# Kernel optimization log

Hardware: AMD Instinct MI355X
Metric: run time of the kernel (lower is better)

The kernel has to match this reference:

```python
import math
import jax, jax.numpy as jnp
from jax import lax
import numpy as np

B_, H_, W_, C_ = 4, 64, 64, 96
DSTATE, DCONV, EXPAND = 16, 3, 2.0
DI = int(EXPAND * C_)            # d_inner = 192
RANK = math.ceil(C_ / 16)        # dt_rank = 6
K = 4                            # 4 scan directions


def setup_inputs() -> dict:
    key = jax.random.key(0)
    ks = jax.random.split(key, 8)
    x = jax.random.normal(ks[0], (B_, H_, W_, C_), jnp.float32)
    in_proj_w = jax.random.normal(ks[1], (2 * DI, C_), jnp.float32) * 0.02
    conv_w = jax.random.normal(ks[2], (DI, 1, DCONV, DCONV), jnp.float32) * 0.1
    conv_b = jnp.zeros((DI,), jnp.float32)
    x_proj_w = jax.random.normal(ks[3], (K, RANK + 2 * DSTATE, DI), jnp.float32) * 0.02
    dt_std = RANK ** -0.5
    dt_projs_w = jax.random.uniform(ks[4], (K, DI, RANK), jnp.float32, -dt_std, dt_std)
    # inverse-softplus init of dt bias, as in dt_init
    dt = jnp.exp(jax.random.uniform(ks[5], (K, DI), jnp.float32)
                 * (math.log(0.1) - math.log(1e-3)) + math.log(1e-3))
    dt = jnp.clip(dt, 1e-4, None)
    dt_projs_b = dt + jnp.log(-jnp.expm1(-dt))
    A_logs = jnp.log(jnp.tile(jnp.arange(1, DSTATE + 1, dtype=jnp.float32)[None, :], (K * DI, 1)))
    Ds = jnp.ones((K * DI,), jnp.float32)
    ln_g = jnp.ones((DI,), jnp.float32)
    ln_b = jnp.zeros((DI,), jnp.float32)
    out_proj_w = jax.random.normal(ks[6], (C_, DI), jnp.float32) * 0.02
    return dict(x=x, in_proj_w=in_proj_w, conv_w=conv_w, conv_b=conv_b,
                x_proj_w=x_proj_w, dt_projs_w=dt_projs_w, dt_projs_b=dt_projs_b,
                A_logs=A_logs, Ds=Ds, ln_g=ln_g, ln_b=ln_b, out_proj_w=out_proj_w)


def reference(x, in_proj_w, conv_w, conv_b, x_proj_w, dt_projs_w, dt_projs_b,
              A_logs, Ds, ln_g, ln_b, out_proj_w):
    B, H, W, C = x.shape
    Di, N, L = DI, DSTATE, H * W
    # in_proj -> x, z gate
    xz = jnp.einsum('bhwc,ec->bhwe', x, in_proj_w)
    xh, z = jnp.split(xz, 2, axis=-1)
    # depthwise 3x3 conv + SiLU (NCHW)
    xc = jnp.transpose(xh, (0, 3, 1, 2))
    xc = lax.conv_general_dilated(xc, conv_w, (1, 1), 'SAME', feature_group_count=Di)
    xc = jax.nn.silu(xc + conv_b[None, :, None, None])
    # 4 directional sequences: hw, wh(transposed), and their reverses
    x_flat = xc.reshape(B, Di, L)
    x_tr = jnp.transpose(xc, (0, 1, 3, 2)).reshape(B, Di, L)
    x_hwwh = jnp.stack([x_flat, x_tr], axis=1)                 # B,2,Di,L
    xs = jnp.concatenate([x_hwwh, jnp.flip(x_hwwh, axis=-1)], axis=1)  # B,K,Di,L
    # projections for dt, B, C
    x_dbl = jnp.einsum('bkdl,kcd->bkcl', xs, x_proj_w)
    dts = x_dbl[:, :, :RANK]
    Bs = x_dbl[:, :, RANK:RANK + N]            # B,K,N,L
    Cs = x_dbl[:, :, RANK + N:]                # B,K,N,L
    dts = jnp.einsum('bkrl,kdr->bkdl', dts, dt_projs_w)
    delta = jax.nn.softplus(dts + dt_projs_b[None, :, :, None])  # B,K,Di,L
    A = -jnp.exp(A_logs).reshape(K, Di, N)
    # selective scan over L (sequential recurrence, vectorized over B,K,Di,N)
    u_l = jnp.transpose(xs, (3, 0, 1, 2))      # L,B,K,Di
    d_l = jnp.transpose(delta, (3, 0, 1, 2))   # L,B,K,Di
    B_l = jnp.transpose(Bs, (3, 0, 1, 2))      # L,B,K,N
    C_l = jnp.transpose(Cs, (3, 0, 1, 2))      # L,B,K,N

    def step(h, inp):
        u_t, d_t, b_t, c_t = inp
        dA = jnp.exp(d_t[..., None] * A[None])                  # B,K,Di,N
        h = h * dA + (d_t * u_t)[..., None] * b_t[:, :, None, :]
        y = jnp.einsum('bkdn,bkn->bkd', h, c_t)
        return h, y

    h0 = jnp.zeros((B, K, Di, N), xs.dtype)
    _, ys = lax.scan(step, h0, (u_l, d_l, B_l, C_l))            # L,B,K,Di
    out_y = jnp.transpose(ys, (1, 2, 3, 0)) + xs * Ds.reshape(K, Di)[None, :, :, None]
    # undo direction permutations and sum the 4 streams
    inv_y = jnp.flip(out_y[:, 2:4], axis=-1)
    wh_y = jnp.transpose(out_y[:, 1].reshape(B, Di, W, H), (0, 1, 3, 2)).reshape(B, Di, L)
    invwh_y = jnp.transpose(inv_y[:, 1].reshape(B, Di, W, H), (0, 1, 3, 2)).reshape(B, Di, L)
    y = out_y[:, 0] + inv_y[:, 0] + wh_y + invwh_y              # B,Di,L
    y = jnp.transpose(y, (0, 2, 1)).reshape(B, H, W, Di)
    # out_norm (LayerNorm), gate with SiLU(z), out_proj
    mu = jnp.mean(y, axis=-1, keepdims=True)
    var = jnp.mean(jnp.square(y - mu), axis=-1, keepdims=True)
    y = (y - mu) * lax.rsqrt(var + 1e-5) * ln_g + ln_b
    y = y * jax.nn.silu(z)
    return jnp.einsum('bhwd,cd->bhwc', y, out_proj_w)
```

## Files before the change

### kernel.cpp

```cpp
#include <hip/hip_runtime.h>
#include <math.h>

#define DI 192
#define NS 16
#define LL 4096
#define NC 128
#define CH 32

__device__ __forceinline__ float siluf(float x) {
  return x / (1.f + __expf(-x));
}

__device__ __forceinline__ int row_l(int k, int p) {
  const int q = (k >= 2) ? (4095 - p) : p;
  return (k & 1) ? (((q & 63) << 6) | (q >> 6)) : q;
}

__device__ __forceinline__ int row_stride(int k) {
  return (k == 0) ? 1 : (k == 1) ? 64 : (k == 2) ? -1 : -64;
}

__device__ __forceinline__ void decays16(float w, float* dec) {
  const float w2 = w * w, w4 = w2 * w2, w8 = w4 * w4;
  const float w3 = w2 * w, w5 = w4 * w, w6 = w4 * w2, w7 = w4 * w3;
  dec[0] = w;  dec[1] = w2; dec[2] = w3; dec[3] = w4;
  dec[4] = w5; dec[5] = w6; dec[6] = w7; dec[7] = w8;
  dec[8] = w8 * w;  dec[9] = w8 * w2; dec[10] = w8 * w3; dec[11] = w8 * w4;
  dec[12] = w8 * w5; dec[13] = w8 * w6; dec[14] = w8 * w7; dec[15] = w8 * w8;
}

__device__ __forceinline__ void softplus_w(float x, float& dl, float& w) {
  const float e = __expf(x);
  dl = __logf(1.f + e);
  w = __builtin_amdgcn_rcpf(1.f + e);
}

__global__ __launch_bounds__(256) void k_inproj(
    const float* __restrict__ x, const float* __restrict__ w,
    float* __restrict__ xh, float* __restrict__ z) {
  __shared__ float As[64 * 97];
  __shared__ float Bs[64 * 97];
  const int t = threadIdx.x;
  const int bm = blockIdx.x, bn = blockIdx.y;
  const float* xrow = x + (size_t)bm * 64 * 96;
  const float* wrow = w + (size_t)bn * 64 * 96;
#pragma unroll
  for (int rep = 0; rep < 6; ++rep) {
    int fi = rep * 256 + t;
    int r = fi / 24, kq = (fi - r * 24) * 4;
    float4 av = *reinterpret_cast<const float4*>(xrow + r * 96 + kq);
    As[r * 97 + kq + 0] = av.x; As[r * 97 + kq + 1] = av.y;
    As[r * 97 + kq + 2] = av.z; As[r * 97 + kq + 3] = av.w;
    float4 bv = *reinterpret_cast<const float4*>(wrow + r * 96 + kq);
    Bs[r * 97 + kq + 0] = bv.x; Bs[r * 97 + kq + 1] = bv.y;
    Bs[r * 97 + kq + 2] = bv.z; Bs[r * 97 + kq + 3] = bv.w;
  }
  __syncthreads();
  const int tm = (t >> 4) * 4, tn = (t & 15) * 4;
  float acc[4][4] = {};
  for (int kk = 0; kk < 96; ++kk) {
    float av[4], bv[4];
#pragma unroll
    for (int i = 0; i < 4; ++i) av[i] = As[(tm + i) * 97 + kk];
#pragma unroll
    for (int j = 0; j < 4; ++j) bv[j] = Bs[(tn + j) * 97 + kk];
#pragma unroll
    for (int i = 0; i < 4; ++i)
#pragma unroll
      for (int j = 0; j < 4; ++j) acc[i][j] += av[i] * bv[j];
  }
  const int e0 = bn * 64 + tn;
#pragma unroll
  for (int i = 0; i < 4; ++i) {
    size_t m = (size_t)bm * 64 + tm + i;
    float4 v = make_float4(acc[i][0], acc[i][1], acc[i][2], acc[i][3]);
    if (e0 < DI) *reinterpret_cast<float4*>(xh + m * DI + e0) = v;
    else         *reinterpret_cast<float4*>(z + m * DI + (e0 - DI)) = v;
  }
}

__global__ __launch_bounds__(192) void k_conv(
    const float* __restrict__ xh, const float* __restrict__ cw,
    const float* __restrict__ cb, float* __restrict__ uT0) {
  __shared__ float tile[DI * 65];
  const int h = blockIdx.x, b = blockIdx.y;
  const int d = threadIdx.x;
  float wgt[9];
#pragma unroll
  for (int i = 0; i < 9; ++i) wgt[i] = cw[d * 9 + i];
  const float bias = cb[d];
  const bool hm = (h > 0), hp = (h < 63);
  const float* rowm = xh + ((size_t)(b * 64 + (h - 1)) * 64) * DI + d;
  const float* row0 = xh + ((size_t)(b * 64 + h) * 64) * DI + d;
  const float* rowp = xh + ((size_t)(b * 64 + (h + 1)) * 64) * DI + d;
  float cp0 = 0.f, cp1 = 0.f, cp2 = 0.f;
  float cc0 = hm ? rowm[0] : 0.f;
  float cc1 = row0[0];
  float cc2 = hp ? rowp[0] : 0.f;
  for (int w = 0; w < 64; ++w) {
    float cn0 = 0.f, cn1 = 0.f, cn2 = 0.f;
    if (w < 63) {
      cn0 = hm ? rowm[(w + 1) * DI] : 0.f;
      cn1 = row0[(w + 1) * DI];
      cn2 = hp ? rowp[(w + 1) * DI] : 0.f;
    }
    float acc = bias
      + cp0 * wgt[0] + cc0 * wgt[1] + cn0 * wgt[2]
      + cp1 * wgt[3] + cc1 * wgt[4] + cn1 * wgt[5]
      + cp2 * wgt[6] + cc2 * wgt[7] + cn2 * wgt[8];
    tile[d * 65 + w] = siluf(acc);
    cp0 = cc0; cp1 = cc1; cp2 = cc2;
    cc0 = cn0; cc1 = cn1; cc2 = cn2;
  }
  __syncthreads();
  for (int w = 0; w < 64; ++w) {
    uT0[((size_t)((b * 64 + h) * 64 + w)) * DI + d] = tile[d * 65 + w];
  }
}

__global__ __launch_bounds__(256, 2) void k_xdbl(
    const float* __restrict__ uT0, const float* __restrict__ xpw,
    float* __restrict__ xdbl) {
  __shared__ float X[DI * 64];
  __shared__ float Wl[40 * DI];
  const int cblk = blockIdx.x, k = blockIdx.y, b = blockIdx.z;
  const int t = threadIdx.x;
  {
    const float4* wsrc = reinterpret_cast<const float4*>(xpw + (size_t)k * 38 * DI);
    float4* wdst = reinterpret_cast<float4*>(Wl);
#pragma unroll
    for (int r = 0; r < 8; ++r) {
      int q = r * 256 + t;
      if (q < 1920) wdst[q] = (q < 1824) ? wsrc[q] : make_float4(0.f, 0.f, 0.f, 0.f);
    }
  }
  {
    const int i = t >> 2, q = t & 3;
    const float* urow = uT0 + ((size_t)b * LL + row_l(k, cblk * 64 + i)) * DI;
    const float4* urow4 = reinterpret_cast<const float4*>(urow);
#pragma unroll
    for (int dd = 0; dd < 12; ++dd) {
      float4 v = urow4[dd * 4 + q];
      const int d0 = (dd * 4 + q) * 4;
      X[(d0 + 0) * 64 + i] = v.x;
      X[(d0 + 1) * 64 + i] = v.y;
      X[(d0 + 2) * 64 + i] = v.z;
      X[(d0 + 3) * 64 + i] = v.w;
    }
  }
  __syncthreads();
  const int c2 = t & 31, g = t >> 5;
  float acc[5][2];
#pragma unroll
  for (int j = 0; j < 5; ++j) { acc[j][0] = 0.f; acc[j][1] = 0.f; }
  for (int dq = 0; dq < 48; ++dq) {
    float4 w[5];
#pragma unroll
    for (int j = 0; j < 5; ++j)
      w[j] = *reinterpret_cast<const float4*>(&Wl[(g * 5 + j) * DI + dq * 4]);
    float x0[4], x1[4];
#pragma unroll
    for (int e = 0; e < 4; ++e) {
      x0[e] = X[(dq * 4 + e) * 64 + c2];
      x1[e] = X[(dq * 4 + e) * 64 + c2 + 32];
    }
#pragma unroll
    for (int j = 0; j < 5; ++j) {
      acc[j][0] += w[j].x * x0[0] + w[j].y * x0[1] + w[j].z * x0[2] + w[j].w * x0[3];
      acc[j][1] += w[j].x * x1[0] + w[j].y * x1[1] + w[j].z * x1[2] + w[j].w * x1[3];
    }
  }
  __syncthreads();
  float* O = X;
#pragma unroll
  for (int j = 0; j < 5; ++j) {
    const int co = g * 5 + j;
    O[(c2 +  0) * 40 + co] = acc[j][0];
    O[(c2 + 32) * 40 + co] = acc[j][1];
  }
  __syncthreads();
  {
    const int bk = b * 4 + k;
    const float4* O4 = reinterpret_cast<const float4*>(O);
    float4* dst4 = reinterpret_cast<float4*>(xdbl + ((size_t)(bk * 64 + cblk) * 64) * 40);
#pragma unroll
    for (int r = 0; r < 3; ++r) {
      int idx = r * 256 + t;
      if (idx < 640) dst4[idx] = O4[idx];
    }
  }
}

__global__ __launch_bounds__(192, 6) void k_scan1(
    const float* __restrict__ uT0, const float* __restrict__ xdbl,
    const float* __restrict__ dtw, const float* __restrict__ dtb,
    float* __restrict__ hbuf, float* __restrict__ sumd) {
  __shared__ float Sl[CH * 40];
  const int c = blockIdx.x, k = blockIdx.y, b = blockIdx.z;
  const int d = threadIdx.x;
  const int kd = k * DI + d;
  const int bk = b * 4 + k;
  {
    const float4* src4 = reinterpret_cast<const float4*>(
        xdbl + ((size_t)bk * LL + c * CH) * 40);
    float4* dst4 = reinterpret_cast<float4*>(Sl);
#pragma unroll
    for (int r = 0; r < 2; ++r) {
      int idx = r * 192 + d;
      if (idx < 320) dst4[idx] = src4[idx];
    }
  }
  float wdt[6];
#pragma unroll
  for (int r = 0; r < 6; ++r) wdt[r] = dtw[kd * 6 + r];
  const float bdt = dtb[kd];
  float h[NS];
#pragma unroll
  for (int n = 0; n < NS; ++n) h[n] = 0.f;
  float sd = 0.f;
  __syncthreads();
  const ptrdiff_t dr = (ptrdiff_t)row_stride(k) * DI;
  const float* up = uT0 + ((size_t)b * LL + row_l(k, c * CH)) * DI + d;
  float uA = *up;
  for (int i = 0; i < CH; ++i) {
    const float uB = (i + 1 < CH) ? up[dr] : 0.f;
    const float* Sr = &Sl[i * 40];
    const float4 q0 = *reinterpret_cast<const float4*>(Sr + 0);
    const float4 q1 = *reinterpret_cast<const float4*>(Sr + 4);
    const float4 q2 = *reinterpret_cast<const float4*>(Sr + 8);
    const float4 q3 = *reinterpret_cast<const float4*>(Sr + 12);
    const float4 q4 = *reinterpret_cast<const float4*>(Sr + 16);
    const float4 q5 = *reinterpret_cast<const float4*>(Sr + 20);
    const float dl0 = bdt + q0.x * wdt[0] + q0.y * wdt[1] + q0.z * wdt[2]
                          + q0.w * wdt[3] + q1.x * wdt[4] + q1.y * wdt[5];
    float dl, w;
    softplus_w(dl0, dl, w);
    sd += dl;
    const float du = dl * uA;
    float dec[NS];
    decays16(w, dec);
    const float fB[16] = {q1.z, q1.w, q2.x, q2.y, q2.z, q2.w, q3.x, q3.y,
                          q3.z, q3.w, q4.x, q4.y, q4.z, q4.w, q5.x, q5.y};
#pragma unroll
    for (int n = 0; n < NS; ++n)
      h[n] = h[n] * dec[n] + du * fB[n];
    up += dr;
    uA = uB;
  }
  const size_t hb = (size_t)(bk * NC + c) * NS;
#pragma unroll
  for (int n = 0; n < NS; ++n) hbuf[(hb + n) * DI + d] = h[n];
  sumd[(size_t)(bk * NC + c) * DI + d] = sd;
}

__global__ __launch_bounds__(256, 2) void k_scan2(
    const float* __restrict__ sumd, float* __restrict__ hbuf) {
  const int bid = blockIdx.x;
  const int bk = bid / 12, r = bid % 12;
  const int n = (r / 3) * 4 + (threadIdx.x >> 6);
  const int d = (r % 3) * 64 + (threadIdx.x & 63);
  const float An = -(float)(n + 1);
  float h = 0.f;
#define HIDX(cc) (((size_t)(bk * NC + (cc)) * NS + n) * DI + d)
#define SIDX(cc) ((size_t)(bk * NC + (cc)) * DI + d)
  float hA = hbuf[HIDX(0)], sA = sumd[SIDX(0)];
  float hB, sB;
  for (int cc = 0; cc < NC; cc += 2) {
    hB = hbuf[HIDX(cc + 1)]; sB = sumd[SIDX(cc + 1)];
    {
      const float wdec = __expf(An * sA);
      hbuf[HIDX(cc)] = h;
      h = h * wdec + hA;
    }
    if (cc + 2 < NC) { hA = hbuf[HIDX(cc + 2)]; sA = sumd[SIDX(cc + 2)]; }
    {
      const float wdec = __expf(An * sB);
      hbuf[HIDX(cc + 1)] = h;
      h = h * wdec + hB;
    }
  }
#undef HIDX
#undef SIDX
}

template <bool ACCUM>
__global__ __launch_bounds__(192, 4) void k_scan3(
    const float* __restrict__ uT0, const float* __restrict__ xdbl,
    const float* __restrict__ dtw, const float* __restrict__ dtb,
    const float* __restrict__ hbuf,
    const float* __restrict__ Dsv, int kbase,
    float* __restrict__ yb0, float* __restrict__ yb1,
    float* __restrict__ yb2, float* __restrict__ yb3) {
  __shared__ float Sl[CH * 40];
  const int c = blockIdx.x, b = blockIdx.z;
  const int k = kbase + (int)blockIdx.y;
  const int d = threadIdx.x;
  const int kd = k * DI + d;
  const int bk = b * 4 + k;
  float* ybuf = (k == 0) ? yb0 : (k == 1) ? yb1 : (k == 2) ? yb2 : yb3;
  {
    const float4* src4 = reinterpret_cast<const float4*>(
        xdbl + ((size_t)bk * LL + c * CH) * 40);
    float4* dst4 = reinterpret_cast<float4*>(Sl);
#pragma unroll
    for (int r = 0; r < 2; ++r) {
      int idx = r * 192 + d;
      if (idx < 320) dst4[idx] = src4[idx];
    }
  }
  float wdt[6];
#pragma unroll
  for (int r = 0; r < 6; ++r) wdt[r] = dtw[kd * 6 + r];
  const float bdt = dtb[kd];
  const float Dv = Dsv[kd];
  float h[NS];
  {
    const size_t hb = (size_t)(bk * NC + c) * NS;
#pragma unroll
    for (int n = 0; n < NS; ++n) h[n] = hbuf[(hb + n) * DI + d];
  }
  __syncthreads();
  const ptrdiff_t dr = (ptrdiff_t)row_stride(k) * DI;
  const size_t base = ((size_t)b * LL + row_l(k, c * CH)) * DI + d;
  const float* up = uT0 + base;
  float* yp = ybuf + base;
  float uA = *up;
  float yoA = ACCUM ? *yp : 0.f;
  for (int i = 0; i < CH; ++i) {
    float uB = 0.f, yoB = 0.f;
    if (i + 1 < CH) {
      uB = up[dr];
      if (ACCUM) yoB = yp[dr];
    }
    const float* Sr = &Sl[i * 40];
    const float4 q0 = *reinterpret_cast<const float4*>(Sr + 0);
    const float4 q1 = *reinterpret_cast<const float4*>(Sr + 4);
    const float4 q2 = *reinterpret_cast<const float4*>(Sr + 8);
    const float4 q3 = *reinterpret_cast<const float4*>(Sr + 12);
    const float4 q4 = *reinterpret_cast<const float4*>(Sr + 16);
    const float4 q5 = *reinterpret_cast<const float4*>(Sr + 20);
    const float4 q6 = *reinterpret_cast<const float4*>(Sr + 24);
    const float4 q7 = *reinterpret_cast<const float4*>(Sr + 28);
    const float4 q8 = *reinterpret_cast<const float4*>(Sr + 32);
    const float4 q9 = *reinterpret_cast<const float4*>(Sr + 36);
    const float dl0 = bdt + q0.x * wdt[0] + q0.y * wdt[1] + q0.z * wdt[2]
                          + q0.w * wdt[3] + q1.x * wdt[4] + q1.y * wdt[5];
    float dl, w;
    softplus_w(dl0, dl, w);
    const float du = dl * uA;
    float yv = Dv * uA;
    float dec[NS];
    decays16(w, dec);
    const float fB[16] = {q1.z, q1.w, q2.x, q2.y, q2.z, q2.w, q3.x, q3.y,
                          q3.z, q3.w, q4.x, q4.y, q4.z, q4.w, q5.x, q5.y};
    const float fC[16] = {q5.z, q5.w, q6.x, q6.y, q6.z, q6.w, q7.x, q7.y,
                          q7.z, q7.w, q8.x, q8.y, q8.z, q8.w, q9.x, q9.y};
#pragma unroll
    for (int n = 0; n < NS; ++n) {
      h[n] = h[n] * dec[n] + du * fB[n];
      yv += h[n] * fC[n];
    }
    if (ACCUM) *yp = yoA + yv;
    else       *yp = yv;
    up += dr; yp += dr;
    uA = uB; yoA = yoB;
  }
}

__global__ __launch_bounds__(256) void k_lnout(
    const float* __restrict__ y0, const float* __restrict__ y1,
    const float* __restrict__ y2, const float* __restrict__ y3,
    int ny,
    const float* __restrict__ z,
    const float* __restrict__ lng, const float* __restrict__ lnb,
    const float* __restrict__ opw, float* __restrict__ out) {
  __shared__ float ytile[64 * 193];
  __shared__ float Wl[96 * DI];
  const int pt = blockIdx.x, b = blockIdx.y;
  const int t = threadIdx.x;
  {
    const float4* wsrc = reinterpret_cast<const float4*>(opw);
    float4* wdst = reinterpret_cast<float4*>(Wl);
#pragma unroll
    for (int r = 0; r < 18; ++r) wdst[r * 256 + t] = wsrc[r * 256 + t];
  }
  {
    const int c = t >> 2, q = t & 3;
    const size_t row = ((size_t)b * LL + pt * 64 + c) * DI;
    const float4* r0 = reinterpret_cast<const float4*>(y0 + row);
    const float4* r1 = reinterpret_cast<const float4*>(y1 + row);
    const float4* r2 = reinterpret_cast<const float4*>(y2 + row);
    const float4* r3 = reinterpret_cast<const float4*>(y3 + row);
#pragma unroll
    for (int dd = 0; dd < 12; ++dd) {
      float4 a = r0[dd * 4 + q];
      float4 bb = r1[dd * 4 + q];
      float vx = a.x + bb.x, vy = a.y + bb.y, vz = a.z + bb.z, vw = a.w + bb.w;
      if (ny == 4) {
        float4 cvv = r2[dd * 4 + q];
        float4 dv = r3[dd * 4 + q];
        vx += cvv.x + dv.x; vy += cvv.y + dv.y;
        vz += cvv.z + dv.z; vw += cvv.w + dv.w;
      }
      const int d0 = (dd * 4 + q) * 4;
      ytile[c * 193 + d0 + 0] = vx;
      ytile[c * 193 + d0 + 1] = vy;
      ytile[c * 193 + d0 + 2] = vz;
      ytile[c * 193 + d0 + 3] = vw;
    }
  }
  __syncthreads();
  {
    const int p = t >> 2, qq = t & 3;
    float s = 0.f, s2 = 0.f;
    for (int j = 0; j < 48; ++j) {
      float v = ytile[p * 193 + qq * 48 + j];
      s += v; s2 += v * v;
    }
    s += __shfl_xor(s, 1, 64);  s += __shfl_xor(s, 2, 64);
    s2 += __shfl_xor(s2, 1, 64); s2 += __shfl_xor(s2, 2, 64);
    const float mu = s * (1.f / 192.f);
    const float var = s2 * (1.f / 192.f) - mu * mu;
    const float rstd = rsqrtf(var + 1e-5f);
    const size_t prow = ((size_t)b * LL + pt * 64 + p) * DI;
    for (int j = 0; j < 48; ++j) {
      int d = qq * 48 + j;
      float v = (ytile[p * 193 + d] - mu) * rstd * lng[d] + lnb[d];
      float zv = z[prow + d];
      v *= siluf(zv);
      ytile[p * 193 + d] = v;
    }
  }
  __syncthreads();
  float acc[24];
#pragma unroll
  for (int j = 0; j < 24; ++j) acc[j] = 0.f;
  const int p2 = t & 63, gq = t >> 6;
  for (int dq = 0; dq < 48; ++dq) {
    float xv[4];
#pragma unroll
    for (int e = 0; e < 4; ++e) xv[e] = ytile[p2 * 193 + dq * 4 + e];
#pragma unroll
    for (int j = 0; j < 24; ++j) {
      const float4 wv = *reinterpret_cast<const float4*>(&Wl[(gq * 24 + j) * DI + dq * 4]);
      acc[j] += wv.x * xv[0] + wv.y * xv[1] + wv.z * xv[2] + wv.w * xv[3];
    }
  }
  __syncthreads();
  float* l2 = ytile;
#pragma unroll
  for (int j = 0; j < 24; ++j) l2[p2 * 97 + gq * 24 + j] = acc[j];
  __syncthreads();
  for (int rr = 0; rr < 24; ++rr) {
    int idx = rr * 256 + t;
    int pp = idx / 96, cc = idx - pp * 96;
    out[((size_t)b * LL + pt * 64 + pp) * 96 + cc] = l2[pp * 97 + cc];
  }
}

extern "C" void kernel_launch(void* const* d_in, const int* in_sizes, int n_in,
                              void* d_out, int out_size, void* d_ws, size_t ws_size,
                              hipStream_t stream) {
  const float* x          = (const float*)d_in[0];
  const float* in_proj_w  = (const float*)d_in[1];
  const float* conv_w     = (const float*)d_in[2];
  const float* conv_b     = (const float*)d_in[3];
  const float* x_proj_w   = (const float*)d_in[4];
  const float* dt_projs_w = (const float*)d_in[5];
  const float* dt_projs_b = (const float*)d_in[6];
  const float* Ds         = (const float*)d_in[8];
  const float* ln_g       = (const float*)d_in[9];
  const float* ln_b       = (const float*)d_in[10];
  const float* out_proj_w = (const float*)d_in[11];
  float* out = (float*)d_out;
  float* ws = (float*)d_ws;
  float* xh   = ws;
  float* z    = ws +  3145728;
  float* uT0  = ws +  6291456;
  float* xdbl = ws +  9437184;
  float* hbuf = ws + 12058624;
  float* y1   = ws + 18350080;
  float* y2   = ws + 21495808;
  float* y3   = ws + 24641536;
  float* sumd = xh;
  float* y0   = xh;
  const bool planA = ws_size >= (size_t)27787264 * 4;

  k_inproj<<<dim3(256, 6), dim3(256), 0, stream>>>(x, in_proj_w, xh, z);
  k_conv<<<dim3(64, 4), dim3(192), 0, stream>>>(xh, conv_w, conv_b, uT0);
  k_xdbl<<<dim3(64, 4, 4), dim3(256), 0, stream>>>(uT0, x_proj_w, xdbl);
  k_scan1<<<dim3(NC, 4, 4), dim3(192), 0, stream>>>(uT0, xdbl,
      dt_projs_w, dt_projs_b, hbuf, sumd);
  k_scan2<<<dim3(192), dim3(256), 0, stream>>>(sumd, hbuf);
  if (planA) {
    k_scan3<false><<<dim3(NC, 4, 4), dim3(192), 0, stream>>>(uT0, xdbl,
        dt_projs_w, dt_projs_b, hbuf, Ds, 0, y0, y1, y2, y3);
    k_lnout<<<dim3(64, 4), dim3(256), 0, stream>>>(y0, y1, y2, y3, 4, z,
        ln_g, ln_b, out_proj_w, out);
  } else {
    k_scan3<false><<<dim3(NC, 2, 4), dim3(192), 0, stream>>>(uT0, xdbl,
        dt_projs_w, dt_projs_b, hbuf, Ds, 0, y0, y1, y0, y1);
    k_scan3<true><<<dim3(NC, 2, 4), dim3(192), 0, stream>>>(uT0, xdbl,
        dt_projs_w, dt_projs_b, hbuf, Ds, 2, y0, y1, y0, y1);
    k_lnout<<<dim3(64, 4), dim3(256), 0, stream>>>(y0, y1, y0, y1, 2, z,
        ln_g, ln_b, out_proj_w, out);
  }
}
```

Measured before the change: 220.2 us.

## Stream scan records from global into registers with double buffering, drop LDS staging

The chunked scan kernels no longer stage the per-chunk x_dbl records into shared memory behind a barrier. Each thread now loads the records for the next step straight from global into a register double buffer while it computes the current step, and the u and y prefetch is widened to match. k_scan3 splits the C-dot into four partial sums to shorten the dependency chain, and k_scan2 prefetches four chunks at a time instead of two. The cost is higher register pressure, reflected in lower launch-bounds occupancy, and redundant per-thread global loads of the same broadcast data, which rely on caching.

```diff
diff --git a/kernel.cpp b/kernel.cpp
--- a/kernel.cpp
+++ b/kernel.cpp
@@ -191,25 +191,16 @@
   }
 }
 
-__global__ __launch_bounds__(192, 6) void k_scan1(
+__global__ __launch_bounds__(192, 5) void k_scan1(
     const float* __restrict__ uT0, const float* __restrict__ xdbl,
     const float* __restrict__ dtw, const float* __restrict__ dtb,
     float* __restrict__ hbuf, float* __restrict__ sumd) {
-  __shared__ float Sl[CH * 40];
   const int c = blockIdx.x, k = blockIdx.y, b = blockIdx.z;
   const int d = threadIdx.x;
   const int kd = k * DI + d;
   const int bk = b * 4 + k;
-  {
-    const float4* src4 = reinterpret_cast<const float4*>(
-        xdbl + ((size_t)bk * LL + c * CH) * 40);
-    float4* dst4 = reinterpret_cast<float4*>(Sl);
-#pragma unroll
-    for (int r = 0; r < 2; ++r) {
-      int idx = r * 192 + d;
-      if (idx < 320) dst4[idx] = src4[idx];
-    }
-  }
+  const float4* Rp = reinterpret_cast<const float4*>(
+      xdbl + ((size_t)bk * LL + c * CH) * 40);
   float wdt[6];
 #pragma unroll
   for (int r = 0; r < 6; ++r) wdt[r] = dtw[kd * 6 + r];
@@ -218,35 +209,47 @@
 #pragma unroll
   for (int n = 0; n < NS; ++n) h[n] = 0.f;
   float sd = 0.f;
-  __syncthreads();
   const ptrdiff_t dr = (ptrdiff_t)row_stride(k) * DI;
   const float* up = uT0 + ((size_t)b * LL + row_l(k, c * CH)) * DI + d;
-  float uA = *up;
-  for (int i = 0; i < CH; ++i) {
-    const float uB = (i + 1 < CH) ? up[dr] : 0.f;
-    const float* Sr = &Sl[i * 40];
-    const float4 q0 = *reinterpret_cast<const float4*>(Sr + 0);
-    const float4 q1 = *reinterpret_cast<const float4*>(Sr + 4);
-    const float4 q2 = *reinterpret_cast<const float4*>(Sr + 8);
-    const float4 q3 = *reinterpret_cast<const float4*>(Sr + 12);
-    const float4 q4 = *reinterpret_cast<const float4*>(Sr + 16);
-    const float4 q5 = *reinterpret_cast<const float4*>(Sr + 20);
-    const float dl0 = bdt + q0.x * wdt[0] + q0.y * wdt[1] + q0.z * wdt[2]
-                          + q0.w * wdt[3] + q1.x * wdt[4] + q1.y * wdt[5];
-    float dl, w;
-    softplus_w(dl0, dl, w);
-    sd += dl;
-    const float du = dl * uA;
-    float dec[NS];
-    decays16(w, dec);
-    const float fB[16] = {q1.z, q1.w, q2.x, q2.y, q2.z, q2.w, q3.x, q3.y,
-                          q3.z, q3.w, q4.x, q4.y, q4.z, q4.w, q5.x, q5.y};
-#pragma unroll
-    for (int n = 0; n < NS; ++n)
-      h[n] = h[n] * dec[n] + du * fB[n];
-    up += dr;
-    uA = uB;
-  }
+  float recA[24], recB[24];
+
+#define LOADR1(dst, ii) do {                                           \
+    _Pragma("unroll")                                                  \
+    for (int q = 0; q < 6; ++q)                                        \
+      *reinterpret_cast<float4*>(&dst[q * 4]) = Rp[(ii) * 10 + q];     \
+  } while (0)
+
+#define STEP1(rec, uu) do {                                            \
+    const float s0_ = bdt + rec[0] * wdt[0] + rec[1] * wdt[1]          \
+                          + rec[2] * wdt[2];                           \
+    const float s1_ = rec[3] * wdt[3] + rec[4] * wdt[4]                \
+                    + rec[5] * wdt[5];                                 \
+    float dl, w;                                                       \
+    softplus_w(s0_ + s1_, dl, w);                                      \
+    sd += dl;                                                          \
+    const float du = dl * (uu);                                        \
+    float dec[NS];                                                     \
+    decays16(w, dec);                                                  \
+    _Pragma("unroll")                                                  \
+    for (int n = 0; n < NS; ++n)                                       \
+      h[n] = h[n] * dec[n] + du * rec[6 + n];                          \
+  } while (0)
+
+  LOADR1(recA, 0);
+  float u0 = up[0];
+  float u1 = up[dr];
+  for (int i = 0; i < CH; i += 2) {
+    if (i + 1 < CH) LOADR1(recB, i + 1);
+    float un0 = (i + 2 < CH) ? up[2 * dr] : 0.f;
+    STEP1(recA, u0);
+    if (i + 2 < CH) LOADR1(recA, i + 2);
+    float un1 = (i + 3 < CH) ? up[3 * dr] : 0.f;
+    STEP1(recB, u1);
+    u0 = un0; u1 = un1; up += 2 * dr;
+  }
+#undef LOADR1
+#undef STEP1
+
   const size_t hb = (size_t)(bk * NC + c) * NS;
 #pragma unroll
   for (int n = 0; n < NS; ++n) hbuf[(hb + n) * DI + d] = h[n];
@@ -263,51 +266,49 @@
   float h = 0.f;
 #define HIDX(cc) (((size_t)(bk * NC + (cc)) * NS + n) * DI + d)
 #define SIDX(cc) ((size_t)(bk * NC + (cc)) * DI + d)
-  float hA = hbuf[HIDX(0)], sA = sumd[SIDX(0)];
-  float hB, sB;
-  for (int cc = 0; cc < NC; cc += 2) {
-    hB = hbuf[HIDX(cc + 1)]; sB = sumd[SIDX(cc + 1)];
-    {
-      const float wdec = __expf(An * sA);
-      hbuf[HIDX(cc)] = h;
-      h = h * wdec + hA;
-    }
-    if (cc + 2 < NC) { hA = hbuf[HIDX(cc + 2)]; sA = sumd[SIDX(cc + 2)]; }
-    {
-      const float wdec = __expf(An * sB);
-      hbuf[HIDX(cc + 1)] = h;
-      h = h * wdec + hB;
-    }
+  float hA[4], sA[4];
+#pragma unroll
+  for (int j = 0; j < 4; ++j) { hA[j] = hbuf[HIDX(j)]; sA[j] = sumd[SIDX(j)]; }
+  for (int cc = 0; cc < NC; cc += 4) {
+    float hB[4], sB[4];
+    if (cc + 4 < NC) {
+#pragma unroll
+      for (int j = 0; j < 4; ++j) {
+        hB[j] = hbuf[HIDX(cc + 4 + j)];
+        sB[j] = sumd[SIDX(cc + 4 + j)];
+      }
+    }
+    float wd[4];
+#pragma unroll
+    for (int j = 0; j < 4; ++j) wd[j] = __expf(An * sA[j]);
+#pragma unroll
+    for (int j = 0; j < 4; ++j) {
+      hbuf[HIDX(cc + j)] = h;
+      h = h * wd[j] + hA[j];
+    }
+#pragma unroll
+    for (int j = 0; j < 4; ++j) { hA[j] = hB[j]; sA[j] = sB[j]; }
   }
 #undef HIDX
 #undef SIDX
 }
 
 template <bool ACCUM>
-__global__ __launch_bounds__(192, 4) void k_scan3(
+__global__ __launch_bounds__(192, 3) void k_scan3(
     const float* __restrict__ uT0, const float* __restrict__ xdbl,
     const float* __restrict__ dtw, const float* __restrict__ dtb,
     const float* __restrict__ hbuf,
     const float* __restrict__ Dsv, int kbase,
     float* __restrict__ yb0, float* __restrict__ yb1,
     float* __restrict__ yb2, float* __restrict__ yb3) {
-  __shared__ float Sl[CH * 40];
   const int c = blockIdx.x, b = blockIdx.z;
   const int k = kbase + (int)blockIdx.y;
   const int d = threadIdx.x;
   const int kd = k * DI + d;
   const int bk = b * 4 + k;
   float* ybuf = (k == 0) ? yb0 : (k == 1) ? yb1 : (k == 2) ? yb2 : yb3;
-  {
-    const float4* src4 = reinterpret_cast<const float4*>(
-        xdbl + ((size_t)bk * LL + c * CH) * 40);
-    float4* dst4 = reinterpret_cast<float4*>(Sl);
-#pragma unroll
-    for (int r = 0; r < 2; ++r) {
-      int idx = r * 192 + d;
-      if (idx < 320) dst4[idx] = src4[idx];
-    }
-  }
+  const float4* Rp = reinterpret_cast<const float4*>(
+      xdbl + ((size_t)bk * LL + c * CH) * 40);
   float wdt[6];
 #pragma unroll
   for (int r = 0; r < 6; ++r) wdt[r] = dtw[kd * 6 + r];
@@ -319,52 +320,61 @@
 #pragma unroll
     for (int n = 0; n < NS; ++n) h[n] = hbuf[(hb + n) * DI + d];
   }
-  __syncthreads();
   const ptrdiff_t dr = (ptrdiff_t)row_stride(k) * DI;
   const size_t base = ((size_t)b * LL + row_l(k, c * CH)) * DI + d;
   const float* up = uT0 + base;
   float* yp = ybuf + base;
-  float uA = *up;
-  float yoA = ACCUM ? *yp : 0.f;
-  for (int i = 0; i < CH; ++i) {
-    float uB = 0.f, yoB = 0.f;
-    if (i + 1 < CH) {
-      uB = up[dr];
-      if (ACCUM) yoB = yp[dr];
-    }
-    const float* Sr = &Sl[i * 40];
-    const float4 q0 = *reinterpret_cast<const float4*>(Sr + 0);
-    const float4 q1 = *reinterpret_cast<const float4*>(Sr + 4);
-    const float4 q2 = *reinterpret_cast<const float4*>(Sr + 8);
-    const float4 q3 = *reinterpret_cast<const float4*>(Sr + 12);
-    const float4 q4 = *reinterpret_cast<const float4*>(Sr + 16);
-    const float4 q5 = *reinterpret_cast<const float4*>(Sr + 20);
-    const float4 q6 = *reinterpret_cast<const float4*>(Sr + 24);
-    const float4 q7 = *reinterpret_cast<const float4*>(Sr + 28);
-    const float4 q8 = *reinterpret_cast<const float4*>(Sr + 32);
-    const float4 q9 = *reinterpret_cast<const float4*>(Sr + 36);
-    const float dl0 = bdt + q0.x * wdt[0] + q0.y * wdt[1] + q0.z * wdt[2]
-                          + q0.w * wdt[3] + q1.x * wdt[4] + q1.y * wdt[5];
-    float dl, w;
-    softplus_w(dl0, dl, w);
-    const float du = dl * uA;
-    float yv = Dv * uA;
-    float dec[NS];
-    decays16(w, dec);
-    const float fB[16] = {q1.z, q1.w, q2.x, q2.y, q2.z, q2.w, q3.x, q3.y,
-                          q3.z, q3.w, q4.x, q4.y, q4.z, q4.w, q5.x, q5.y};
-    const float fC[16] = {q5.z, q5.w, q6.x, q6.y, q6.z, q6.w, q7.x, q7.y,
-                          q7.z, q7.w, q8.x, q8.y, q8.z, q8.w, q9.x, q9.y};
-#pragma unroll
-    for (int n = 0; n < NS; ++n) {
-      h[n] = h[n] * dec[n] + du * fB[n];
-      yv += h[n] * fC[n];
-    }
-    if (ACCUM) *yp = yoA + yv;
-    else       *yp = yv;
-    up += dr; yp += dr;
-    uA = uB; yoA = yoB;
-  }
+  float recA[40], recB[40];
+
+#define LOADR3(dst, ii) do {                                           \
+    _Pragma("unroll")                                                  \
+    for (int q = 0; q < 10; ++q)                                       \
+      *reinterpret_cast<float4*>(&dst[q * 4]) = Rp[(ii) * 10 + q];     \
+  } while (0)
+
+#define STEP3(rec, uu, yo, yoff) do {                                  \
+    const float s0_ = bdt + rec[0] * wdt[0] + rec[1] * wdt[1]          \
+                          + rec[2] * wdt[2];                           \
+    const float s1_ = rec[3] * wdt[3] + rec[4] * wdt[4]                \
+                    + rec[5] * wdt[5];                                 \
+    float dl, w;                                                       \
+    softplus_w(s0_ + s1_, dl, w);                                      \
+    const float du = dl * (uu);                                        \
+    float dec[NS];                                                     \
+    decays16(w, dec);                                                  \
+    float yv0 = Dv * (uu), yv1 = 0.f, yv2 = 0.f, yv3 = 0.f;            \
+    _Pragma("unroll")                                                  \
+    for (int n = 0; n < NS; ++n) {                                     \
+      h[n] = h[n] * dec[n] + du * rec[6 + n];                          \
+      const float t_ = h[n] * rec[22 + n];                             \
+      if ((n & 3) == 0) yv0 += t_;                                     \
+      else if ((n & 3) == 1) yv1 += t_;                                \
+      else if ((n & 3) == 2) yv2 += t_;                                \
+      else yv3 += t_;                                                  \
+    }                                                                  \
+    const float yv_ = (yv0 + yv1) + (yv2 + yv3);                       \
+    yp[yoff] = ACCUM ? ((yo) + yv_) : yv_;                             \
+  } while (0)
+
+  LOADR3(recA, 0);
+  float u0 = up[0];
+  float u1 = up[dr];
+  float yo0 = ACCUM ? yp[0] : 0.f;
+  float yo1 = ACCUM ? yp[dr] : 0.f;
+  for (int i = 0; i < CH; i += 2) {
+    if (i + 1 < CH) LOADR3(recB, i + 1);
+    float un0 = 0.f, yn0 = 0.f;
+    if (i + 2 < CH) { un0 = up[2 * dr]; if (ACCUM) yn0 = yp[2 * dr]; }
+    STEP3(recA, u0, yo0, 0);
+    if (i + 2 < CH) LOADR3(recA, i + 2);
+    float un1 = 0.f, yn1 = 0.f;
+    if (i + 3 < CH) { un1 = up[3 * dr]; if (ACCUM) yn1 = yp[3 * dr]; }
+    STEP3(recB, u1, yo1, dr);
+    u0 = un0; u1 = un1; yo0 = yn0; yo1 = yn1;
+    up += 2 * dr; yp += 2 * dr;
+  }
+#undef LOADR3
+#undef STEP3
 }
 
 __global__ __launch_bounds__(256) void k_lnout(
```

After: 243.8 us. 1.11x slower.

## Map one wave per chunk covering all channels in scan kernels

Applied to the files above, without the earlier changes.

Restructures the chunked scan kernels so that each 64-lane wavefront handles one chunk and processes three channels per lane, with four chunks per 256-thread block. Each lane reads the shared B/C/dt row once and reuses it across its three channels, which cuts LDS reads and per-block staging overhead. The output reduction is split into four partial sums to shorten the dependency chain, and the inter-chunk scan2 prefetches four chunks ahead. In exchange, register pressure rises (three 16-entry state vectors per thread), which lowers occupancy and leaves fewer blocks to spread across CUs.

```diff
diff --git a/kernel.cpp b/kernel.cpp
--- a/kernel.cpp
+++ b/kernel.cpp
@@ -191,66 +191,84 @@
   }
 }
 
-__global__ __launch_bounds__(192, 6) void k_scan1(
+#define SCAN_QLOAD6(Sr)                                                \
+    const float4 q0 = *reinterpret_cast<const float4*>((Sr) + 0);      \
+    const float4 q1 = *reinterpret_cast<const float4*>((Sr) + 4);      \
+    const float4 q2 = *reinterpret_cast<const float4*>((Sr) + 8);      \
+    const float4 q3 = *reinterpret_cast<const float4*>((Sr) + 12);     \
+    const float4 q4 = *reinterpret_cast<const float4*>((Sr) + 16);     \
+    const float4 q5 = *reinterpret_cast<const float4*>((Sr) + 20);
+
+__global__ __launch_bounds__(256, 3) void k_scan1(
     const float* __restrict__ uT0, const float* __restrict__ xdbl,
     const float* __restrict__ dtw, const float* __restrict__ dtb,
     float* __restrict__ hbuf, float* __restrict__ sumd) {
-  __shared__ float Sl[CH * 40];
-  const int c = blockIdx.x, k = blockIdx.y, b = blockIdx.z;
-  const int d = threadIdx.x;
-  const int kd = k * DI + d;
+  __shared__ float Sl[4][CH * 40];
+  const int cblk = blockIdx.x, k = blockIdx.y, b = blockIdx.z;
+  const int wv = threadIdx.x >> 6, lane = threadIdx.x & 63;
+  const int c = cblk * 4 + wv;
   const int bk = b * 4 + k;
   {
-    const float4* src4 = reinterpret_cast<const float4*>(
+    const float4* src = reinterpret_cast<const float4*>(
         xdbl + ((size_t)bk * LL + c * CH) * 40);
-    float4* dst4 = reinterpret_cast<float4*>(Sl);
-#pragma unroll
-    for (int r = 0; r < 2; ++r) {
-      int idx = r * 192 + d;
-      if (idx < 320) dst4[idx] = src4[idx];
-    }
-  }
-  float wdt[6];
-#pragma unroll
-  for (int r = 0; r < 6; ++r) wdt[r] = dtw[kd * 6 + r];
-  const float bdt = dtb[kd];
-  float h[NS];
-#pragma unroll
-  for (int n = 0; n < NS; ++n) h[n] = 0.f;
-  float sd = 0.f;
+    float4* dst = reinterpret_cast<float4*>(Sl[wv]);
+#pragma unroll
+    for (int r = 0; r < 5; ++r) dst[r * 64 + lane] = src[r * 64 + lane];
+  }
+  float wdt[3][6], bdt[3];
+#pragma unroll
+  for (int s = 0; s < 3; ++s) {
+    const int kd = k * DI + lane + 64 * s;
+#pragma unroll
+    for (int r = 0; r < 6; ++r) wdt[s][r] = dtw[kd * 6 + r];
+    bdt[s] = dtb[kd];
+  }
+  float h[3][NS];
+#pragma unroll
+  for (int s = 0; s < 3; ++s)
+#pragma unroll
+    for (int n = 0; n < NS; ++n) h[s][n] = 0.f;
+  float sd[3] = {0.f, 0.f, 0.f};
   __syncthreads();
   const ptrdiff_t dr = (ptrdiff_t)row_stride(k) * DI;
-  const float* up = uT0 + ((size_t)b * LL + row_l(k, c * CH)) * DI + d;
-  float uA = *up;
+  const float* up = uT0 + ((size_t)b * LL + row_l(k, c * CH)) * DI + lane;
+  float u0 = up[0], u1 = up[64], u2 = up[128];
   for (int i = 0; i < CH; ++i) {
-    const float uB = (i + 1 < CH) ? up[dr] : 0.f;
-    const float* Sr = &Sl[i * 40];
-    const float4 q0 = *reinterpret_cast<const float4*>(Sr + 0);
-    const float4 q1 = *reinterpret_cast<const float4*>(Sr + 4);
-    const float4 q2 = *reinterpret_cast<const float4*>(Sr + 8);
-    const float4 q3 = *reinterpret_cast<const float4*>(Sr + 12);
-    const float4 q4 = *reinterpret_cast<const float4*>(Sr + 16);
-    const float4 q5 = *reinterpret_cast<const float4*>(Sr + 20);
-    const float dl0 = bdt + q0.x * wdt[0] + q0.y * wdt[1] + q0.z * wdt[2]
-                          + q0.w * wdt[3] + q1.x * wdt[4] + q1.y * wdt[5];
-    float dl, w;
-    softplus_w(dl0, dl, w);
-    sd += dl;
-    const float du = dl * uA;
-    float dec[NS];
-    decays16(w, dec);
+    float un0 = 0.f, un1 = 0.f, un2 = 0.f;
+    if (i + 1 < CH) { un0 = up[dr]; un1 = up[dr + 64]; un2 = up[dr + 128]; }
+    const float* Sr = &Sl[wv][i * 40];
+    SCAN_QLOAD6(Sr)
     const float fB[16] = {q1.z, q1.w, q2.x, q2.y, q2.z, q2.w, q3.x, q3.y,
                           q3.z, q3.w, q4.x, q4.y, q4.z, q4.w, q5.x, q5.y};
-#pragma unroll
-    for (int n = 0; n < NS; ++n)
-      h[n] = h[n] * dec[n] + du * fB[n];
+    const float uu[3] = {u0, u1, u2};
+#pragma unroll
+    for (int s = 0; s < 3; ++s) {
+      const float dl0 = bdt[s] + q0.x * wdt[s][0] + q0.y * wdt[s][1]
+          + q0.z * wdt[s][2] + q0.w * wdt[s][3] + q1.x * wdt[s][4]
+          + q1.y * wdt[s][5];
+      float dl, w;
+      softplus_w(dl0, dl, w);
+      sd[s] += dl;
+      const float du = dl * uu[s];
+      float dec[NS];
+      decays16(w, dec);
+#pragma unroll
+      for (int n = 0; n < NS; ++n)
+        h[s][n] = h[s][n] * dec[n] + du * fB[n];
+    }
     up += dr;
-    uA = uB;
+    u0 = un0; u1 = un1; u2 = un2;
   }
   const size_t hb = (size_t)(bk * NC + c) * NS;
 #pragma unroll
-  for (int n = 0; n < NS; ++n) hbuf[(hb + n) * DI + d] = h[n];
-  sumd[(size_t)(bk * NC + c) * DI + d] = sd;
+  for (int n = 0; n < NS; ++n) {
+#pragma unroll
+    for (int s = 0; s < 3; ++s)
+      hbuf[(hb + n) * DI + lane + 64 * s] = h[s][n];
+  }
+#pragma unroll
+  for (int s = 0; s < 3; ++s)
+    sumd[(size_t)(bk * NC + c) * DI + lane + 64 * s] = sd[s];
 }
 
 __global__ __launch_bounds__(256, 2) void k_scan2(
@@ -263,107 +281,120 @@
   float h = 0.f;
 #define HIDX(cc) (((size_t)(bk * NC + (cc)) * NS + n) * DI + d)
 #define SIDX(cc) ((size_t)(bk * NC + (cc)) * DI + d)
-  float hA = hbuf[HIDX(0)], sA = sumd[SIDX(0)];
-  float hB, sB;
-  for (int cc = 0; cc < NC; cc += 2) {
-    hB = hbuf[HIDX(cc + 1)]; sB = sumd[SIDX(cc + 1)];
-    {
-      const float wdec = __expf(An * sA);
-      hbuf[HIDX(cc)] = h;
-      h = h * wdec + hA;
-    }
-    if (cc + 2 < NC) { hA = hbuf[HIDX(cc + 2)]; sA = sumd[SIDX(cc + 2)]; }
-    {
-      const float wdec = __expf(An * sB);
-      hbuf[HIDX(cc + 1)] = h;
-      h = h * wdec + hB;
-    }
+  float hA[4], sA[4];
+#pragma unroll
+  for (int j = 0; j < 4; ++j) { hA[j] = hbuf[HIDX(j)]; sA[j] = sumd[SIDX(j)]; }
+  for (int cc = 0; cc < NC; cc += 4) {
+    float hB[4], sB[4];
+    if (cc + 4 < NC) {
+#pragma unroll
+      for (int j = 0; j < 4; ++j) {
+        hB[j] = hbuf[HIDX(cc + 4 + j)];
+        sB[j] = sumd[SIDX(cc + 4 + j)];
+      }
+    }
+    float wd[4];
+#pragma unroll
+    for (int j = 0; j < 4; ++j) wd[j] = __expf(An * sA[j]);
+#pragma unroll
+    for (int j = 0; j < 4; ++j) {
+      hbuf[HIDX(cc + j)] = h;
+      h = h * wd[j] + hA[j];
+    }
+#pragma unroll
+    for (int j = 0; j < 4; ++j) { hA[j] = hB[j]; sA[j] = sB[j]; }
   }
 #undef HIDX
 #undef SIDX
 }
 
 template <bool ACCUM>
-__global__ __launch_bounds__(192, 4) void k_scan3(
+__global__ __launch_bounds__(256, 3) void k_scan3(
     const float* __restrict__ uT0, const float* __restrict__ xdbl,
     const float* __restrict__ dtw, const float* __restrict__ dtb,
     const float* __restrict__ hbuf,
     const float* __restrict__ Dsv, int kbase,
     float* __restrict__ yb0, float* __restrict__ yb1,
     float* __restrict__ yb2, float* __restrict__ yb3) {
-  __shared__ float Sl[CH * 40];
-  const int c = blockIdx.x, b = blockIdx.z;
+  __shared__ float Sl[4][CH * 40];
+  const int cblk = blockIdx.x, b = blockIdx.z;
   const int k = kbase + (int)blockIdx.y;
-  const int d = threadIdx.x;
-  const int kd = k * DI + d;
+  const int wv = threadIdx.x >> 6, lane = threadIdx.x & 63;
+  const int c = cblk * 4 + wv;
   const int bk = b * 4 + k;
   float* ybuf = (k == 0) ? yb0 : (k == 1) ? yb1 : (k == 2) ? yb2 : yb3;
   {
-    const float4* src4 = reinterpret_cast<const float4*>(
+    const float4* src = reinterpret_cast<const float4*>(
         xdbl + ((size_t)bk * LL + c * CH) * 40);
-    float4* dst4 = reinterpret_cast<float4*>(Sl);
-#pragma unroll
-    for (int r = 0; r < 2; ++r) {
-      int idx = r * 192 + d;
-      if (idx < 320) dst4[idx] = src4[idx];
-    }
-  }
-  float wdt[6];
-#pragma unroll
-  for (int r = 0; r < 6; ++r) wdt[r] = dtw[kd * 6 + r];
-  const float bdt = dtb[kd];
-  const float Dv = Dsv[kd];
-  float h[NS];
+    float4* dst = reinterpret_cast<float4*>(Sl[wv]);
+#pragma unroll
+    for (int r = 0; r < 5; ++r) dst[r * 64 + lane] = src[r * 64 + lane];
+  }
+  float wdt[3][6], bdt[3], Dv[3];
+#pragma unroll
+  for (int s = 0; s < 3; ++s) {
+    const int kd = k * DI + lane + 64 * s;
+#pragma unroll
+    for (int r = 0; r < 6; ++r) wdt[s][r] = dtw[kd * 6 + r];
+    bdt[s] = dtb[kd];
+    Dv[s] = Dsv[kd];
+  }
+  float h[3][NS];
   {
     const size_t hb = (size_t)(bk * NC + c) * NS;
 #pragma unroll
-    for (int n = 0; n < NS; ++n) h[n] = hbuf[(hb + n) * DI + d];
+    for (int n = 0; n < NS; ++n) {
+#pragma unroll
+      for (int s = 0; s < 3; ++s)
+        h[s][n] = hbuf[(hb + n) * DI + lane + 64 * s];
+    }
   }
   __syncthreads();
   const ptrdiff_t dr = (ptrdiff_t)row_stride(k) * DI;
-  const size_t base = ((size_t)b * LL + row_l(k, c * CH)) * DI + d;
+  const size_t base = ((size_t)b * LL + row_l(k, c * CH)) * DI + lane;
   const float* up = uT0 + base;
   float* yp = ybuf + base;
-  float uA = *up;
-  float yoA = ACCUM ? *yp : 0.f;
+  float u0 = up[0], u1 = up[64], u2 = up[128];
   for (int i = 0; i < CH; ++i) {
-    float uB = 0.f, yoB = 0.f;
-    if (i + 1 < CH) {
-      uB = up[dr];
-      if (ACCUM) yoB = yp[dr];
-    }
-    const float* Sr = &Sl[i * 40];
-    const float4 q0 = *reinterpret_cast<const float4*>(Sr + 0);
-    const float4 q1 = *reinterpret_cast<const float4*>(Sr + 4);
-    const float4 q2 = *reinterpret_cast<const float4*>(Sr + 8);
-    const float4 q3 = *reinterpret_cast<const float4*>(Sr + 12);
-    const float4 q4 = *reinterpret_cast<const float4*>(Sr + 16);
-    const float4 q5 = *reinterpret_cast<const float4*>(Sr + 20);
+    float un0 = 0.f, un1 = 0.f, un2 = 0.f;
+    if (i + 1 < CH) { un0 = up[dr]; un1 = up[dr + 64]; un2 = up[dr + 128]; }
+    const float* Sr = &Sl[wv][i * 40];
+    SCAN_QLOAD6(Sr)
     const float4 q6 = *reinterpret_cast<const float4*>(Sr + 24);
     const float4 q7 = *reinterpret_cast<const float4*>(Sr + 28);
     const float4 q8 = *reinterpret_cast<const float4*>(Sr + 32);
     const float4 q9 = *reinterpret_cast<const float4*>(Sr + 36);
-    const float dl0 = bdt + q0.x * wdt[0] + q0.y * wdt[1] + q0.z * wdt[2]
-                          + q0.w * wdt[3] + q1.x * wdt[4] + q1.y * wdt[5];
-    float dl, w;
-    softplus_w(dl0, dl, w);
-    const float du = dl * uA;
-    float yv = Dv * uA;
-    float dec[NS];
-    decays16(w, dec);
     const float fB[16] = {q1.z, q1.w, q2.x, q2.y, q2.z, q2.w, q3.x, q3.y,
                           q3.z, q3.w, q4.x, q4.y, q4.z, q4.w, q5.x, q5.y};
     const float fC[16] = {q5.z, q5.w, q6.x, q6.y, q6.z, q6.w, q7.x, q7.y,
                           q7.z, q7.w, q8.x, q8.y, q8.z, q8.w, q9.x, q9.y};
-#pragma unroll
-    for (int n = 0; n < NS; ++n) {
-      h[n] = h[n] * dec[n] + du * fB[n];
-      yv += h[n] * fC[n];
-    }
-    if (ACCUM) *yp = yoA + yv;
-    else       *yp = yv;
+    const float uu[3] = {u0, u1, u2};
+#pragma unroll
+    for (int s = 0; s < 3; ++s) {
+      const float dl0 = bdt[s] + q0.x * wdt[s][0] + q0.y * wdt[s][1]
+          + q0.z * wdt[s][2] + q0.w * wdt[s][3] + q1.x * wdt[s][4]
+          + q1.y * wdt[s][5];
+      float dl, w;
+      softplus_w(dl0, dl, w);
+      const float du = dl * uu[s];
+      float dec[NS];
+      decays16(w, dec);
+      float yv0 = Dv[s] * uu[s], yv1 = 0.f, yv2 = 0.f, yv3 = 0.f;
+#pragma unroll
+      for (int n = 0; n < NS; ++n) {
+        h[s][n] = h[s][n] * dec[n] + du * fB[n];
+        const float t_ = h[s][n] * fC[n];
+        if ((n & 3) == 0) yv0 += t_;
+        else if ((n & 3) == 1) yv1 += t_;
+        else if ((n & 3) == 2) yv2 += t_;
+        else yv3 += t_;
+      }
+      float yv = (yv0 + yv1) + (yv2 + yv3);
+      if (ACCUM) yv += yp[s * 64];
+      yp[s * 64] = yv;
+    }
     up += dr; yp += dr;
-    uA = uB; yoA = yoB;
+    u0 = un0; u1 = un1; u2 = un2;
   }
 }
 
@@ -489,18 +520,18 @@
   k_inproj<<<dim3(256, 6), dim3(256), 0, stream>>>(x, in_proj_w, xh, z);
   k_conv<<<dim3(64, 4), dim3(192), 0, stream>>>(xh, conv_w, conv_b, uT0);
   k_xdbl<<<dim3(64, 4, 4), dim3(256), 0, stream>>>(uT0, x_proj_w, xdbl);
-  k_scan1<<<dim3(NC, 4, 4), dim3(192), 0, stream>>>(uT0, xdbl,
+  k_scan1<<<dim3(NC / 4, 4, 4), dim3(256), 0, stream>>>(uT0, xdbl,
       dt_projs_w, dt_projs_b, hbuf, sumd);
   k_scan2<<<dim3(192), dim3(256), 0, stream>>>(sumd, hbuf);
   if (planA) {
-    k_scan3<false><<<dim3(NC, 4, 4), dim3(192), 0, stream>>>(uT0, xdbl,
+    k_scan3<false><<<dim3(NC / 4, 4, 4), dim3(256), 0, stream>>>(uT0, xdbl,
         dt_projs_w, dt_projs_b, hbuf, Ds, 0, y0, y1, y2, y3);
     k_lnout<<<dim3(64, 4), dim3(256), 0, stream>>>(y0, y1, y2, y3, 4, z,
         ln_g, ln_b, out_proj_w, out);
   } else {
-    k_scan3<false><<<dim3(NC, 2, 4), dim3(192), 0, stream>>>(uT0, xdbl,
+    k_scan3<false><<<dim3(NC / 4, 2, 4), dim3(256), 0, stream>>>(uT0, xdbl,
         dt_projs_w, dt_projs_b, hbuf, Ds, 0, y0, y1, y0, y1);
-    k_scan3<true><<<dim3(NC, 2, 4), dim3(192), 0, stream>>>(uT0, xdbl,
+    k_scan3<true><<<dim3(NC / 4, 2, 4), dim3(256), 0, stream>>>(uT0, xdbl,
         dt_projs_w, dt_projs_b, hbuf, Ds, 2, y0, y1, y0, y1);
     k_lnout<<<dim3(64, 4), dim3(256), 0, stream>>>(y0, y1, y0, y1, 2, z,
         ln_g, ln_b, out_proj_w, out);
```

Result: no change. 216.2 us (-1.8%).
